# Kernel tuning notes

Hardware: AMD Instinct MI355X
Metric: run time of the kernel (lower is better)

The kernel has to match this reference:

```python
import jax, jax.numpy as jnp
import numpy as np

N, M, D, DV = 8192, 8192, 64, 64

def setup_inputs() -> dict:
    key = jax.random.key(0)
    kq, kk, kv = jax.random.split(key, 3)
    Q = jax.random.normal(kq, (N, D), dtype=jnp.float32)
    K = jax.random.normal(kk, (M, D), dtype=jnp.float32)
    V = jax.random.normal(kv, (M, DV), dtype=jnp.float32)
    return {"Q": Q, "K": K, "V": V}

def reference(Q, K, V):
    d = K.shape[-1]
    scores = jnp.einsum('nd,md->nm', Q, K) / jnp.sqrt(jnp.float32(d))  # [N, M]
    attn = jax.nn.softmax(scores, axis=-1)
    return attn @ V  # [N, DV]
```

## Files before the change

kernel.cpp:

```cpp
#include <hip/hip_runtime.h>


#define NQ 8192
#define NK 8192

typedef float f32x4 __attribute__((ext_vector_type(4)));
typedef short short8 __attribute__((ext_vector_type(8)));
union U4 { uint4 u; short8 s; };

#define MFMA16 __builtin_amdgcn_mfma_f32_16x16x32_bf16

__device__ __forceinline__ unsigned pk2(float a, float b) {
    unsigned ua = __builtin_bit_cast(unsigned, a);
    unsigned ub = __builtin_bit_cast(unsigned, b);
    ua = (ua + 0x7FFFu + ((ua >> 16) & 1u)) >> 16;
    ub = (ub + 0x7FFFu + ((ub >> 16) & 1u)) & 0xFFFF0000u;
    return ua | ub;
}

__device__ __forceinline__ unsigned pkt(float a, float b) {
    return __builtin_amdgcn_perm(__builtin_bit_cast(unsigned, b),
                                 __builtin_bit_cast(unsigned, a), 0x07060302u);
}

__device__ __forceinline__ void async16(const uint4* g, uint4* l) {
    __builtin_amdgcn_global_load_lds(
        (const __attribute__((address_space(1))) void*)g,
        (__attribute__((address_space(3))) void*)l, 16, 0, 0);
}

__global__ __launch_bounds__(256)
void prepass(const float* __restrict__ Kg, const float* __restrict__ Vg,
             uint4* __restrict__ Kb4, uint4* __restrict__ Vt4) {
    __shared__ float ld[64 * 33];
    const int t = threadIdx.x, b = blockIdx.x;

    if (b < 256) {
        const int kl = t >> 3, dg = t & 7;
        const int e = kl & 1, i16 = kl >> 1, h = dg >> 2, q = dg & 3;
        const float* gp = Kg + (size_t)(b * 32 + kl) * 64 + dg * 8;
        float4 f0 = *(const float4*)gp;
        float4 f1 = *(const float4*)(gp + 4);
        uint4 o = make_uint4(pk2(f0.x, f0.y), pk2(f0.z, f0.w),
                             pk2(f1.x, f1.y), pk2(f1.z, f1.w));
        Kb4[(size_t)(b * 4 + e * 2 + h) * 64 + i16 * 4 + q] = o;
    } else {
        const int c = b - 256;
        {
            const int key = t >> 3, dg = t & 7;
            const float* gp = Vg + (size_t)(c * 32 + key) * 64 + dg * 8;
            float4 f0 = *(const float4*)gp;
            float4 f1 = *(const float4*)(gp + 4);
            ld[(dg * 8 + 0) * 33 + key] = f0.x;
            ld[(dg * 8 + 1) * 33 + key] = f0.y;
            ld[(dg * 8 + 2) * 33 + key] = f0.z;
            ld[(dg * 8 + 3) * 33 + key] = f0.w;
            ld[(dg * 8 + 4) * 33 + key] = f1.x;
            ld[(dg * 8 + 5) * 33 + key] = f1.y;
            ld[(dg * 8 + 6) * 33 + key] = f1.z;
            ld[(dg * 8 + 7) * 33 + key] = f1.w;
        }
        __syncthreads();
        {
            const int dim = t >> 2, kq = t & 3;
            const int dt = dim >> 4, i16 = dim & 15;
            float v[8];
            #pragma unroll
            for (int j = 0; j < 8; ++j) v[j] = ld[dim * 33 + kq * 8 + j];
            uint4 o = make_uint4(pk2(v[0], v[1]), pk2(v[2], v[3]),
                                 pk2(v[4], v[5]), pk2(v[6], v[7]));
            Vt4[(size_t)(c * 4 + dt) * 64 + i16 * 4 + kq] = o;
        }
    }
}

__global__ __launch_bounds__(1024)
void attn_main(const float* __restrict__ Qg,
               const uint4* __restrict__ Kb4,
               const uint4* __restrict__ Vt4,
               float* __restrict__ Opart,
               float* __restrict__ Lpart) {
    __shared__ uint4 shb4[8192];
    float* sF = (float*)shb4;
    unsigned* shu = (unsigned*)shb4;

    const int t = threadIdx.x, w = t >> 6, lane = t & 63;
    const int q = lane >> 4, i16 = lane & 15;
    const int rh = w >> 3;
    const int kc = w & 7;
    const int bid = blockIdx.x;
    const int kh = bid & 1;
    const int rg = bid >> 1;
    const int qb0 = rg * 64;
    const int lsl = i16 * 4 + q;
    const int phase = rg & 15;

    const float SCL = 0.18033688011112042f;
    short8 aq[2][2];
    #pragma unroll
    for (int rt = 0; rt < 2; ++rt) {
        const float* qp = Qg + (size_t)(qb0 + rh * 32 + rt * 16 + i16) * 64 + q * 8;
        float4 f0 = *(const float4*)(qp);
        float4 f1 = *(const float4*)(qp + 4);
        U4 u;
        u.u = make_uint4(pk2(f0.x * SCL, f0.y * SCL), pk2(f0.z * SCL, f0.w * SCL),
                         pk2(f1.x * SCL, f1.y * SCL), pk2(f1.z * SCL, f1.w * SCL));
        aq[rt][0] = u.s;
        f0 = *(const float4*)(qp + 32);
        f1 = *(const float4*)(qp + 36);
        u.u = make_uint4(pk2(f0.x * SCL, f0.y * SCL), pk2(f0.z * SCL, f0.w * SCL),
                         pk2(f1.x * SCL, f1.y * SCL), pk2(f1.z * SCL, f1.w * SCL));
        aq[rt][1] = u.s;
    }

    f32x4 acc[2][4];
    float lsum[2][4];
    #pragma unroll
    for (int rt = 0; rt < 2; ++rt) {
        #pragma unroll
        for (int dt = 0; dt < 4; ++dt) { acc[rt][dt][0]=0.f; acc[rt][dt][1]=0.f; acc[rt][dt][2]=0.f; acc[rt][dt][3]=0.f; }
        #pragma unroll
        for (int r = 0; r < 4; ++r) lsum[rt][r] = 0.f;
    }

    const int tpw = ((i16 >> 2) & 1) + 2 * q + 32 * (i16 >> 3);
    const int pp  = i16 & 3;
    const int tpr = (q & 1) + 2 * ((i16 >> 2) & 3) + 8 * (i16 & 3) + 32 * (q >> 1);

    uint4 vf[4];

#define DMA_K(TT, B)                                                          \
    do {                                                                      \
        const int Tp = ((TT) + phase) & 15;                                   \
        _Pragma("unroll")                                                     \
        for (int i = 0; i < 2; ++i) {                                         \
            const int o = w * 128 + i * 64;                                   \
            const int cg = (kh << 7) + Tp * 8 + (o >> 8);                     \
            async16(Kb4 + (size_t)(cg * 4 + ((o >> 6) & 3)) * 64 + lane,      \
                    shb4 + (B) * 2048 + o);                                   \
        }                                                                     \
    } while (0)

#define LOADV(TT)                                                             \
    do {                                                                      \
        const int Tp = ((TT) + phase) & 15;                                   \
        const int cg = (kh << 7) + Tp * 8 + kc;                               \
        _Pragma("unroll")                                                     \
        for (int dt = 0; dt < 4; ++dt)                                        \
            vf[dt] = Vt4[(size_t)(cg * 4 + dt) * 64 + lsl];                   \
    } while (0)

#define QKEXP(B, PAR)                                                         \
    do {                                                                      \
        const uint4* kbuf = shb4 + (B) * 2048 + kc * 256;                     \
        U4 u0, u1, u2, u3;                                                    \
        u0.u = kbuf[0 * 64 + lsl];                                            \
        u1.u = kbuf[1 * 64 + lsl];                                            \
        u2.u = kbuf[2 * 64 + lsl];                                            \
        u3.u = kbuf[3 * 64 + lsl];                                            \
        _Pragma("unroll")                                                     \
        for (int rt = 0; rt < 2; ++rt) {                                      \
            f32x4 s0, s1;                                                     \
            s0[0]=-16.f; s0[1]=-16.f; s0[2]=-16.f; s0[3]=-16.f;               \
            s1[0]=-16.f; s1[1]=-16.f; s1[2]=-16.f; s1[3]=-16.f;               \
            s0 = MFMA16(aq[rt][0], u0.s, s0, 0, 0, 0);                        \
            s0 = MFMA16(aq[rt][1], u1.s, s0, 0, 0, 0);                        \
            s1 = MFMA16(aq[rt][0], u2.s, s1, 0, 0, 0);                        \
            s1 = MFMA16(aq[rt][1], u3.s, s1, 0, 0, 0);                        \
            const int rbase = (4096 + (((w * 2 + rt) * 2) + (PAR)) * 64) * 4; \
            _Pragma("unroll")                                                 \
            for (int r = 0; r < 4; ++r) {                                     \
                float p0 = __builtin_amdgcn_exp2f(s0[r]);                     \
                float p1 = __builtin_amdgcn_exp2f(s1[r]);                     \
                lsum[rt][r] += p0;                                            \
                lsum[rt][r] += p1;                                            \
                shu[rbase + (tpw + 8 * r) * 4 + pp] = pkt(p0, p1);            \
            }                                                                 \
        }                                                                     \
    } while (0)

#define PVS(PAR)                                                              \
    do {                                                                      \
        U4 ap0, ap1;                                                          \
        ap0.u = shb4[4096 + (((w * 2 + 0) * 2) + (PAR)) * 64 + tpr];          \
        ap1.u = shb4[4096 + (((w * 2 + 1) * 2) + (PAR)) * 64 + tpr];          \
        _Pragma("unroll")                                                     \
        for (int dt = 0; dt < 4; ++dt) {                                      \
            U4 bv; bv.u = vf[dt];                                             \
            acc[0][dt] = MFMA16(ap0.s, bv.s, acc[0][dt], 0, 0, 0);            \
            acc[1][dt] = MFMA16(ap1.s, bv.s, acc[1][dt], 0, 0, 0);            \
        }                                                                     \
    } while (0)

    DMA_K(0, 0);
    __syncthreads();
    DMA_K(1, 1);
    QKEXP(0, 0);
    LOADV(0);
    __syncthreads();
    #pragma unroll 1
    for (int tt = 1; tt < 15; tt += 2) {
        DMA_K(tt + 1, 0);
        QKEXP(1, 1);
        PVS(0);
        LOADV(tt);
        __syncthreads();
        DMA_K(tt + 2, 1);
        QKEXP(0, 0);
        PVS(1);
        LOADV(tt + 1);
        __syncthreads();
    }
    QKEXP(1, 1);
    PVS(0);
    LOADV(15);
    PVS(1);

    #pragma unroll
    for (int rt = 0; rt < 2; ++rt)
        #pragma unroll
        for (int r = 0; r < 4; ++r) {
            float v = lsum[rt][r];
            v += __shfl_xor(v, 1);
            v += __shfl_xor(v, 2);
            v += __shfl_xor(v, 4);
            v += __shfl_xor(v, 8);
            lsum[rt][r] = v;
        }

    __syncthreads();
    #pragma unroll 1
    for (int step = 4; step >= 1; step >>= 1) {
        if (kc >= step && kc < 2 * step) {
            float* base = sF + (rh * 4 + (kc - step)) * 2080;
            #pragma unroll
            for (int rt = 0; rt < 2; ++rt) {
                #pragma unroll
                for (int dt = 0; dt < 4; ++dt)
                    #pragma unroll
                    for (int r = 0; r < 4; ++r)
                        base[(rt * 16 + 4 * q + r) * 64 + dt * 16 + i16] = acc[rt][dt][r];
                if (i16 == 0) {
                    #pragma unroll
                    for (int r = 0; r < 4; ++r) base[2048 + rt * 16 + 4 * q + r] = lsum[rt][r];
                }
            }
        }
        __syncthreads();
        if (kc < step) {
            const float* base = sF + (rh * 4 + kc) * 2080;
            #pragma unroll
            for (int rt = 0; rt < 2; ++rt) {
                #pragma unroll
                for (int dt = 0; dt < 4; ++dt)
                    #pragma unroll
                    for (int r = 0; r < 4; ++r)
                        acc[rt][dt][r] += base[(rt * 16 + 4 * q + r) * 64 + dt * 16 + i16];
                #pragma unroll
                for (int r = 0; r < 4; ++r) lsum[rt][r] += base[2048 + rt * 16 + 4 * q + r];
            }
        }
        __syncthreads();
    }

    if (kc == 0) {
        #pragma unroll
        for (int rt = 0; rt < 2; ++rt) {
            #pragma unroll
            for (int dt = 0; dt < 4; ++dt)
                #pragma unroll
                for (int r = 0; r < 4; ++r) {
                    const int row = qb0 + rh * 32 + rt * 16 + 4 * q + r;
                    Opart[((size_t)kh * 8192 + row) * 64 + dt * 16 + i16] = acc[rt][dt][r];
                }
            if (i16 == 0) {
                #pragma unroll
                for (int r = 0; r < 4; ++r)
                    Lpart[kh * 8192 + qb0 + rh * 32 + rt * 16 + 4 * q + r] = lsum[rt][r];
            }
        }
    }
}

__global__ __launch_bounds__(256)
void merge(const float* __restrict__ Opart, const float* __restrict__ Lpart,
           float* __restrict__ Og) {
    const int idx = blockIdx.x * 256 + threadIdx.x;
    const int row = idx >> 4, seg = idx & 15;
    const float4 a = *(const float4*)(Opart + (size_t)row * 64 + seg * 4);
    const float4 b = *(const float4*)(Opart + ((size_t)8192 + row) * 64 + seg * 4);
    const float inv = 1.0f / (Lpart[row] + Lpart[8192 + row]);
    float4 o;
    o.x = (a.x + b.x) * inv;
    o.y = (a.y + b.y) * inv;
    o.z = (a.z + b.z) * inv;
    o.w = (a.w + b.w) * inv;
    *(float4*)(Og + (size_t)row * 64 + seg * 4) = o;
}

extern "C" void kernel_launch(void* const* d_in, const int* in_sizes, int n_in,
                              void* d_out, int out_size, void* d_ws, size_t ws_size,
                              hipStream_t stream) {
    const float* Q = (const float*)d_in[0];
    const float* K = (const float*)d_in[1];
    const float* V = (const float*)d_in[2];
    float* O = (float*)d_out;
    char* ws = (char*)d_ws;
    uint4* Kb4   = (uint4*)ws;
    uint4* Vt4   = (uint4*)(ws + (1 << 20));
    float* Opart = (float*)(ws + (2 << 20));
    float* Lpart = (float*)(ws + (6 << 20));
    hipLaunchKernelGGL(prepass, dim3(512), dim3(256), 0, stream, K, V, Kb4, Vt4);
    hipLaunchKernelGGL(attn_main, dim3(256), dim3(1024), 0, stream, Q, Kb4, Vt4, Opart, Lpart);
    hipLaunchKernelGGL(merge, dim3(512), dim3(256), 0, stream, Opart, Lpart, O);
}
```

Before: 101.1 us.

## Swap K/V staging: K in registers, V async to LDS, drop block barriers

The main loop now loads each wave's K fragments straight into registers with a double-buffered register set, and streams V tiles asynchronously into double-buffered LDS. Block-wide __syncthreads are replaced by per-wave waitcnt plus sched_barrier, because each wave only reads LDS data it fetched itself. The prepass also writes eight replicated copies of the bf16 K and V so that blocks spread their reads across separate copies, which likely aims to reduce L2/channel contention. In exchange it costs more prepass traffic, a larger workspace, more LDS and more registers. The loop also prefetches tiles past index 15, but the phase-wrapped indexing keeps those reads in bounds.

```diff
diff --git a/kernel.cpp b/kernel.cpp
--- a/kernel.cpp
+++ b/kernel.cpp
@@ -34,18 +34,21 @@
              uint4* __restrict__ Kb4, uint4* __restrict__ Vt4) {
     __shared__ float ld[64 * 33];
     const int t = threadIdx.x, b = blockIdx.x;
-
-    if (b < 256) {
+    const int copy = b & 7, j = b >> 3;
+    uint4* Kc = Kb4 + (size_t)copy * 65536;
+    uint4* Vc = Vt4 + (size_t)copy * 65536;
+
+    if (j < 256) {
         const int kl = t >> 3, dg = t & 7;
         const int e = kl & 1, i16 = kl >> 1, h = dg >> 2, q = dg & 3;
-        const float* gp = Kg + (size_t)(b * 32 + kl) * 64 + dg * 8;
+        const float* gp = Kg + (size_t)(j * 32 + kl) * 64 + dg * 8;
         float4 f0 = *(const float4*)gp;
         float4 f1 = *(const float4*)(gp + 4);
         uint4 o = make_uint4(pk2(f0.x, f0.y), pk2(f0.z, f0.w),
                              pk2(f1.x, f1.y), pk2(f1.z, f1.w));
-        Kb4[(size_t)(b * 4 + e * 2 + h) * 64 + i16 * 4 + q] = o;
+        Kc[(size_t)(j * 4 + e * 2 + h) * 64 + i16 * 4 + q] = o;
     } else {
-        const int c = b - 256;
+        const int c = j - 256;
         {
             const int key = t >> 3, dg = t & 7;
             const float* gp = Vg + (size_t)(c * 32 + key) * 64 + dg * 8;
@@ -66,10 +69,10 @@
             const int dt = dim >> 4, i16 = dim & 15;
             float v[8];
             #pragma unroll
-            for (int j = 0; j < 8; ++j) v[j] = ld[dim * 33 + kq * 8 + j];
+            for (int jj = 0; jj < 8; ++jj) v[jj] = ld[dim * 33 + kq * 8 + jj];
             uint4 o = make_uint4(pk2(v[0], v[1]), pk2(v[2], v[3]),
                                  pk2(v[4], v[5]), pk2(v[6], v[7]));
-            Vt4[(size_t)(c * 4 + dt) * 64 + i16 * 4 + kq] = o;
+            Vc[(size_t)(c * 4 + dt) * 64 + i16 * 4 + kq] = o;
         }
     }
 }
@@ -80,7 +83,7 @@
                const uint4* __restrict__ Vt4,
                float* __restrict__ Opart,
                float* __restrict__ Lpart) {
-    __shared__ uint4 shb4[8192];
+    __shared__ uint4 shb4[10240];
     float* sF = (float*)shb4;
     unsigned* shu = (unsigned*)shb4;
 
@@ -94,6 +97,8 @@
     const int qb0 = rg * 64;
     const int lsl = i16 * 4 + q;
     const int phase = rg & 15;
+    const uint4* Kb = Kb4 + (size_t)(bid & 7) * 65536;
+    const uint4* Vt = Vt4 + (size_t)(bid & 7) * 65536;
 
     const float SCL = 0.18033688011112042f;
     short8 aq[2][2];
@@ -127,37 +132,29 @@
     const int pp  = i16 & 3;
     const int tpr = (q & 1) + 2 * ((i16 >> 2) & 3) + 8 * (i16 & 3) + 32 * (q >> 1);
 
-    uint4 vf[4];
-
-#define DMA_K(TT, B)                                                          \
+    uint4 kfA[4], kfB[4];
+
+#define DMA_V(TT, B)                                                          \
     do {                                                                      \
-        const int Tp = ((TT) + phase) & 15;                                   \
-        _Pragma("unroll")                                                     \
-        for (int i = 0; i < 2; ++i) {                                         \
-            const int o = w * 128 + i * 64;                                   \
-            const int cg = (kh << 7) + Tp * 8 + (o >> 8);                     \
-            async16(Kb4 + (size_t)(cg * 4 + ((o >> 6) & 3)) * 64 + lane,      \
-                    shb4 + (B) * 2048 + o);                                   \
-        }                                                                     \
-    } while (0)
-
-#define LOADV(TT)                                                             \
-    do {                                                                      \
-        const int Tp = ((TT) + phase) & 15;                                   \
-        const int cg = (kh << 7) + Tp * 8 + kc;                               \
+        const int cg = (kh << 7) + ((((TT) + phase) & 15) * 8 + kc);          \
         _Pragma("unroll")                                                     \
         for (int dt = 0; dt < 4; ++dt)                                        \
-            vf[dt] = Vt4[(size_t)(cg * 4 + dt) * 64 + lsl];                   \
+            async16(Vt + (size_t)(cg * 4 + dt) * 64 + lane,                   \
+                    shb4 + (B) * 4096 + w * 256 + dt * 64);                   \
     } while (0)
 
-#define QKEXP(B, PAR)                                                         \
+#define LOADK(TT, KD)                                                         \
     do {                                                                      \
-        const uint4* kbuf = shb4 + (B) * 2048 + kc * 256;                     \
+        const int cg = (kh << 7) + ((((TT) + phase) & 15) * 8 + kc);          \
+        _Pragma("unroll")                                                     \
+        for (int eh = 0; eh < 4; ++eh)                                        \
+            (KD)[eh] = Kb[(size_t)(cg * 4 + eh) * 64 + lsl];                  \
+    } while (0)
+
+#define QKEXP(KD)                                                             \
+    do {                                                                      \
         U4 u0, u1, u2, u3;                                                    \
-        u0.u = kbuf[0 * 64 + lsl];                                            \
-        u1.u = kbuf[1 * 64 + lsl];                                            \
-        u2.u = kbuf[2 * 64 + lsl];                                            \
-        u3.u = kbuf[3 * 64 + lsl];                                            \
+        u0.u = (KD)[0]; u1.u = (KD)[1]; u2.u = (KD)[2]; u3.u = (KD)[3];       \
         _Pragma("unroll")                                                     \
         for (int rt = 0; rt < 2; ++rt) {                                      \
             f32x4 s0, s1;                                                     \
@@ -167,7 +164,7 @@
             s0 = MFMA16(aq[rt][1], u1.s, s0, 0, 0, 0);                        \
             s1 = MFMA16(aq[rt][0], u2.s, s1, 0, 0, 0);                        \
             s1 = MFMA16(aq[rt][1], u3.s, s1, 0, 0, 0);                        \
-            const int rbase = (4096 + (((w * 2 + rt) * 2) + (PAR)) * 64) * 4; \
+            const int rbase = (8192 + (w * 2 + rt) * 64) * 4;                 \
             _Pragma("unroll")                                                 \
             for (int r = 0; r < 4; ++r) {                                     \
                 float p0 = __builtin_amdgcn_exp2f(s0[r]);                     \
@@ -179,42 +176,36 @@
         }                                                                     \
     } while (0)
 
-#define PVS(PAR)                                                              \
+#define PVS(B)                                                                \
     do {                                                                      \
         U4 ap0, ap1;                                                          \
-        ap0.u = shb4[4096 + (((w * 2 + 0) * 2) + (PAR)) * 64 + tpr];          \
-        ap1.u = shb4[4096 + (((w * 2 + 1) * 2) + (PAR)) * 64 + tpr];          \
+        ap0.u = shb4[8192 + (w * 2 + 0) * 64 + tpr];                          \
+        ap1.u = shb4[8192 + (w * 2 + 1) * 64 + tpr];                          \
         _Pragma("unroll")                                                     \
         for (int dt = 0; dt < 4; ++dt) {                                      \
-            U4 bv; bv.u = vf[dt];                                             \
+            U4 bv; bv.u = shb4[(B) * 4096 + w * 256 + dt * 64 + lsl];         \
             acc[0][dt] = MFMA16(ap0.s, bv.s, acc[0][dt], 0, 0, 0);            \
             acc[1][dt] = MFMA16(ap1.s, bv.s, acc[1][dt], 0, 0, 0);            \
         }                                                                     \
     } while (0)
 
-    DMA_K(0, 0);
-    __syncthreads();
-    DMA_K(1, 1);
-    QKEXP(0, 0);
-    LOADV(0);
-    __syncthreads();
+    DMA_V(0, 0); LOADK(0, kfA);
+    DMA_V(1, 1); LOADK(1, kfB);
     #pragma unroll 1
-    for (int tt = 1; tt < 15; tt += 2) {
-        DMA_K(tt + 1, 0);
-        QKEXP(1, 1);
+    for (int tt = 0; tt < 16; tt += 2) {
+        __builtin_amdgcn_s_waitcnt(0x0F78);
+        __builtin_amdgcn_sched_barrier(0);
+        QKEXP(kfA);
         PVS(0);
-        LOADV(tt);
-        __syncthreads();
-        DMA_K(tt + 2, 1);
-        QKEXP(0, 0);
+        __builtin_amdgcn_sched_barrier(0);
+        DMA_V(tt + 2, 0); LOADK(tt + 2, kfA);
+        __builtin_amdgcn_s_waitcnt(0x0F78);
+        __builtin_amdgcn_sched_barrier(0);
+        QKEXP(kfB);
         PVS(1);
-        LOADV(tt + 1);
-        __syncthreads();
-    }
-    QKEXP(1, 1);
-    PVS(0);
-    LOADV(15);
-    PVS(1);
+        __builtin_amdgcn_sched_barrier(0);
+        DMA_V(tt + 3, 1); LOADK(tt + 3, kfB);
+    }
 
     #pragma unroll
     for (int rt = 0; rt < 2; ++rt)
@@ -307,10 +298,10 @@
     float* O = (float*)d_out;
     char* ws = (char*)d_ws;
     uint4* Kb4   = (uint4*)ws;
-    uint4* Vt4   = (uint4*)(ws + (1 << 20));
-    float* Opart = (float*)(ws + (2 << 20));
-    float* Lpart = (float*)(ws + (6 << 20));
-    hipLaunchKernelGGL(prepass, dim3(512), dim3(256), 0, stream, K, V, Kb4, Vt4);
+    uint4* Vt4   = (uint4*)(ws + (8 << 20));
+    float* Opart = (float*)(ws + (16 << 20));
+    float* Lpart = (float*)(ws + (20 << 20));
+    hipLaunchKernelGGL(prepass, dim3(4096), dim3(256), 0, stream, K, V, Kb4, Vt4);
     hipLaunchKernelGGL(attn_main, dim3(256), dim3(1024), 0, stream, Q, Kb4, Vt4, Opart, Lpart);
     hipLaunchKernelGGL(merge, dim3(512), dim3(256), 0, stream, Opart, Lpart, O);
 }
```

Measured after the change: 111.7 us. 1.1x slower.
